# Optimization experiments

Measured on AMD Instinct MI355X. Metric: run time of the kernel, lower is better.

The kernel has to match this reference:

```python
import jax, jax.numpy as jnp
import numpy as np

N_USERS = 100_000
N_ITEMS = 50_000
N_EDGES = 2_000_000
D = 64
ALPHA = 0.5      # tanh-blend coefficient (alpha)
NORM_2 = -1.0    # exponent on back-aggregation degree norm (args.norm_2)


def setup_inputs() -> dict:
    key = jax.random.key(0)
    k1, k2, k3, k4, k5 = jax.random.split(key, 5)
    return {
        "h_user": jax.random.normal(k1, (N_USERS, D), jnp.float32) * 0.1,
        "pretrained_feature": jax.random.normal(k2, (N_ITEMS, D), jnp.float32),
        "edge_w": jax.random.normal(k3, (N_ITEMS, 1), jnp.float32),
        "src_idx": jax.random.randint(k4, (N_EDGES,), 0, N_USERS, dtype=jnp.int32),
        "dst_idx": jax.random.randint(k5, (N_EDGES,), 0, N_ITEMS, dtype=jnp.int32),
    }


def reference(h_user, pretrained_feature, edge_w, src_idx, dst_idx):
    # HGCNLayer.forward: bidirectional copy_src+sum aggregation with degree norm,
    # tanh prompt blend and node-softmax edge weighting.
    ones = jnp.ones((N_EDGES,), h_user.dtype)

    # forward pass user -> item: rst[d] = sum_{(s,d) in E} h_user[s]
    rst = jax.ops.segment_sum(h_user[src_idx], dst_idx, num_segments=N_ITEMS)  # [N_ITEMS, D]
    deg_dst = jnp.clip(jax.ops.segment_sum(ones, dst_idx, num_segments=N_ITEMS), 1.0)

    # alpha * tanh prompt blend
    rst = rst + ALPHA * jnp.tanh(pretrained_feature)
    # edge-prompt softmax scaling (softmax over nodes; see notes)
    rst = jax.nn.softmax(edge_w, axis=0) * rst
    # in-degree^-1 normalization
    rst = rst / deg_dst[:, None]

    # backward pass item -> user: bsrc[s] = sum_{(s,d) in E} rst[d]
    bsrc = jax.ops.segment_sum(rst[dst_idx], src_idx, num_segments=N_USERS)  # [N_USERS, D]
    deg_src = jnp.clip(jax.ops.segment_sum(ones, src_idx, num_segments=N_USERS), 1.0)
    bsrc = bsrc * jnp.power(deg_src, NORM_2)[:, None]
    return bsrc
```

## Files before the change

kernel.cpp:

```cpp
#include <hip/hip_runtime.h>
#include <hip/hip_bf16.h>
#include <math.h>

#define N_USERS 100000
#define N_ITEMS 50000
#define N_EDGES 2000000
#define D 64

#define SEG_SH 14
#define FSEG 8
#define BSEG 4
#define FB2 (98 * FSEG)
#define BB2 (196 * BSEG)
#define NB2 (FB2 + BB2)
#define CHUNK 16384
#define NCHUNK ((N_EDGES + CHUNK - 1) / CHUNK)
#define FWD_WGS 782
#define BWD_WGS 1563
#define CAPC 1024

__device__ __forceinline__ float blo(unsigned u) {
    union { unsigned i; float f; } c; c.i = u << 16; return c.f;
}
__device__ __forceinline__ float bhi(unsigned u) {
    union { unsigned i; float f; } c; c.i = u & 0xFFFF0000u; return c.f;
}
__device__ __forceinline__ unsigned bpack(float x, float y) {
    __hip_bfloat16 a = __float2bfloat16(x), b = __float2bfloat16(y);
    unsigned short ua = *reinterpret_cast<unsigned short*>(&a);
    unsigned short ub = *reinterpret_cast<unsigned short*>(&b);
    return (unsigned)ua | ((unsigned)ub << 16);
}

__global__ __launch_bounds__(256) void h2b_kernel(
    const float2* __restrict__ in, unsigned* __restrict__ out, int n) {
    int stride = gridDim.x * blockDim.x;
    for (int i = blockIdx.x * blockDim.x + threadIdx.x; i < n; i += stride) {
        float2 v = in[i];
        out[i] = bpack(v.x, v.y);
    }
}

__global__ __launch_bounds__(256) void hist_kernel(
    const int* __restrict__ src, const int* __restrict__ dst, int* __restrict__ gh) {
    __shared__ int h[NB2];
    for (int i = threadIdx.x; i < NB2; i += 256) h[i] = 0;
    __syncthreads();
    int stride = gridDim.x * blockDim.x;
    for (int e = blockIdx.x * blockDim.x + threadIdx.x; e < N_EDGES; e += stride) {
        int s = src[e], d = dst[e];
        atomicAdd(&h[(d >> 9) * FSEG + (s >> SEG_SH)], 1);
        atomicAdd(&h[FB2 + (s >> 9) * BSEG + (d >> SEG_SH)], 1);
    }
    __syncthreads();
    for (int i = threadIdx.x; i < NB2; i += 256) {
        int v = h[i];
        if (v) atomicAdd(&gh[i], v);
    }
}

__global__ void scan_excl(const int* __restrict__ in, int* __restrict__ out,
                          int* __restrict__ cur, int n) {
    const int T = 1024, E = 4;
    __shared__ int wsum[16];
    __shared__ int s_carry;
    if (threadIdx.x == 0) s_carry = 0;
    __syncthreads();

    int lane = threadIdx.x & 63;
    int wid  = threadIdx.x >> 6;

    for (int base = 0; base < n; base += T * E) {
        int idx0 = base + threadIdx.x * E;
        int v[E];
        int tot = 0;
#pragma unroll
        for (int e = 0; e < E; e++) {
            int i = idx0 + e;
            v[e] = (i < n) ? in[i] : 0;
            tot += v[e];
        }
        int incl = tot;
#pragma unroll
        for (int off = 1; off < 64; off <<= 1) {
            int t = __shfl_up(incl, off);
            if (lane >= off) incl += t;
        }
        if (lane == 63) wsum[wid] = incl;
        __syncthreads();
        if (wid == 0 && lane < 16) {
            int t = wsum[lane];
            int sc = t;
#pragma unroll
            for (int off = 1; off < 16; off <<= 1) {
                int u = __shfl_up(sc, off);
                if (lane >= off) sc += u;
            }
            wsum[lane] = sc - t;
        }
        __syncthreads();
        int wave_off = wsum[wid];
        int excl = s_carry + wave_off + incl - tot;
#pragma unroll
        for (int e = 0; e < E; e++) {
            int i = idx0 + e;
            if (i < n) { out[i] = excl; cur[i] = excl; }
            excl += v[e];
        }
        __syncthreads();
        if (threadIdx.x == T - 1) s_carry += wave_off + incl;
        __syncthreads();
    }
    if (threadIdx.x == 0) out[n] = s_carry;
}

__global__ __launch_bounds__(256) void binfill_kernel(
    const int* __restrict__ src, const int* __restrict__ dst,
    int* __restrict__ gcur, unsigned* __restrict__ stage) {
    __shared__ int cnt[NB2];
    __shared__ int gbase[NB2];
    __shared__ int lcur[NB2];
    int base = blockIdx.x * CHUNK;
    int nE = N_EDGES - base; if (nE > CHUNK) nE = CHUNK;

    for (int t = threadIdx.x; t < NB2; t += 256) { cnt[t] = 0; lcur[t] = 0; }
    __syncthreads();

    for (int k = threadIdx.x; k < nE; k += 256) {
        int s = src[base + k], d = dst[base + k];
        atomicAdd(&cnt[(d >> 9) * FSEG + (s >> SEG_SH)], 1);
        atomicAdd(&cnt[FB2 + (s >> 9) * BSEG + (d >> SEG_SH)], 1);
    }
    __syncthreads();
    for (int t = threadIdx.x; t < NB2; t += 256) {
        int cv = cnt[t];
        gbase[t] = cv ? atomicAdd(&gcur[t], cv) : 0;
    }
    __syncthreads();
    for (int k = threadIdx.x; k < nE; k += 256) {
        int s = src[base + k], d = dst[base + k];
        int bf = (d >> 9) * FSEG + (s >> SEG_SH);
        int p = atomicAdd(&lcur[bf], 1);
        stage[gbase[bf] + p] = (unsigned)s | ((unsigned)(d & 511) << 17);
        int bb = FB2 + (s >> 9) * BSEG + (d >> SEG_SH);
        int q2 = atomicAdd(&lcur[bb], 1);
        stage[gbase[bb] + q2] = (unsigned)d | ((unsigned)(s & 511) << 16);
    }
}

__global__ void softmax_stats_kernel(const float* __restrict__ w, float* __restrict__ stats) {
    __shared__ float red[16];
    int tid = threadIdx.x, lane = tid & 63, wid = tid >> 6;

    float m = -INFINITY;
    for (int i = tid; i < N_ITEMS; i += 1024) m = fmaxf(m, w[i]);
#pragma unroll
    for (int off = 32; off; off >>= 1) m = fmaxf(m, __shfl_xor(m, off));
    if (lane == 0) red[wid] = m;
    __syncthreads();
    if (tid == 0) {
        float t = red[0];
        for (int k = 1; k < 16; k++) t = fmaxf(t, red[k]);
        red[0] = t;
    }
    __syncthreads();
    m = red[0];
    __syncthreads();

    float s = 0.f;
    for (int i = tid; i < N_ITEMS; i += 1024) s += expf(w[i] - m);
#pragma unroll
    for (int off = 32; off; off >>= 1) s += __shfl_xor(s, off);
    if (lane == 0) red[wid] = s;
    __syncthreads();
    if (tid == 0) {
        float t = 0.f;
        for (int k = 0; k < 16; k++) t += red[k];
        stats[0] = m;
        stats[1] = t;
    }
}

__global__ __launch_bounds__(512) void pass2_fwd_kernel(
    const unsigned* __restrict__ hu16, const float* __restrict__ pf,
    const float* __restrict__ edge_w, const unsigned* __restrict__ stage,
    const int* __restrict__ binoff, const float* __restrict__ stats,
    unsigned* __restrict__ rst16) {
    __shared__ int cnt[64];
    __shared__ int loc[65];
    __shared__ int lcur[64];
    __shared__ int sorted[CAPC];
    int r = blockIdx.x;
    int B = r >> 3, sub = r & 7;
    int tid = threadIdx.x, lane = tid & 63, wv = tid >> 6;
    int q = lane & 31, half = lane >> 5;

    float ax[8], ay[8];
    int dg[8];
#pragma unroll
    for (int j = 0; j < 8; j++) { ax[j] = 0.f; ay[j] = 0.f; dg[j] = 0; }

    for (int seg = 0; seg < FSEG; seg++) {
        int cbeg = binoff[B * FSEG + seg], cend = binoff[B * FSEG + seg + 1];
        if (cbeg == cend) continue;
        if (tid < 64) { cnt[tid] = 0; lcur[tid] = 0; }
        __syncthreads();
        for (int k = cbeg + tid; k < cend; k += 512) {
            unsigned e = stage[k];
            if ((int)(e >> 23) == sub) atomicAdd(&cnt[(e >> 17) & 63], 1);
        }
        __syncthreads();
        if (tid < 64) {
            int v = cnt[tid];
            int incl = v;
#pragma unroll
            for (int off = 1; off < 64; off <<= 1) {
                int t = __shfl_up(incl, off);
                if (tid >= off) incl += t;
            }
            loc[tid] = incl - v;
            if (tid == 63) loc[64] = incl;
        }
        __syncthreads();
        int nf = loc[64];

        if (nf <= CAPC) {
            for (int k = cbeg + tid; k < cend; k += 512) {
                unsigned e = stage[k];
                if ((int)(e >> 23) == sub) {
                    int il = (e >> 17) & 63;
                    int p = atomicAdd(&lcur[il], 1);
                    sorted[loc[il] + p] = (int)(e & 0x1FFFFu);
                }
            }
            __syncthreads();
#pragma unroll
            for (int j = 0; j < 8; j++) {
                int il = wv + 8 * j;
                int a = loc[il], b = loc[il + 1];
                dg[j] += b - a;
                int k = a;
                for (; k + 4 <= b; k += 4) {
                    int s0 = sorted[k + half], s1 = sorted[k + 2 + half];
                    unsigned u0 = hu16[(s0 << 5) + q];
                    unsigned u1 = hu16[(s1 << 5) + q];
                    ax[j] += blo(u0) + blo(u1);
                    ay[j] += bhi(u0) + bhi(u1);
                }
                for (; k + 2 <= b; k += 2) {
                    unsigned u = hu16[(sorted[k + half] << 5) + q];
                    ax[j] += blo(u); ay[j] += bhi(u);
                }
                if (k < b && half == 0) {
                    unsigned u = hu16[(sorted[k] << 5) + q];
                    ax[j] += blo(u); ay[j] += bhi(u);
                }
            }
            __syncthreads();
        } else {
#pragma unroll
            for (int j = 0; j < 8; j++) {
                int il = wv + 8 * j;
                unsigned want = ((unsigned)sub << 6) | (unsigned)il;
                for (int k = cbeg; k < cend; k++) {
                    unsigned e = stage[k];
                    if ((e >> 17) == want) {
                        dg[j]++;
                        if (half == 0) {
                            unsigned u = hu16[((e & 0x1FFFFu) << 5) + q];
                            ax[j] += blo(u); ay[j] += bhi(u);
                        }
                    }
                }
            }
            __syncthreads();
        }
    }

    float m = stats[0], ssum = stats[1];
    const float2* PF2 = (const float2*)pf;
#pragma unroll
    for (int j = 0; j < 8; j++) {
        int il = wv + 8 * j;
        int i = r * 64 + il;
        if (i >= N_ITEMS) continue;
        ax[j] += __shfl_xor(ax[j], 32);
        ay[j] += __shfl_xor(ay[j], 32);
        if (half == 0) {
            float deg = (float)dg[j];
            if (deg < 1.f) deg = 1.f;
            float sc = expf(edge_w[i] - m) / (ssum * deg);
            float2 pv = PF2[(size_t)i * 32 + q];
            float vx = (ax[j] + 0.5f * tanhf(pv.x)) * sc;
            float vy = (ay[j] + 0.5f * tanhf(pv.y)) * sc;
            rst16[(size_t)i * 32 + q] = bpack(vx, vy);
        }
    }
}

__global__ __launch_bounds__(512) void pass2_bwd_kernel(
    const unsigned* __restrict__ rst16, const unsigned* __restrict__ stage,
    const int* __restrict__ binoff, float* __restrict__ out) {
    __shared__ int cnt[64];
    __shared__ int loc[65];
    __shared__ int lcur[64];
    __shared__ int sorted[CAPC];
    int r = blockIdx.x;
    int B = r >> 3, sub = r & 7;
    int tid = threadIdx.x, lane = tid & 63, wv = tid >> 6;
    int q = lane & 31, half = lane >> 5;

    float ax[8], ay[8];
    int dg[8];
#pragma unroll
    for (int j = 0; j < 8; j++) { ax[j] = 0.f; ay[j] = 0.f; dg[j] = 0; }

    for (int seg = 0; seg < BSEG; seg++) {
        int cbeg = binoff[FB2 + B * BSEG + seg], cend = binoff[FB2 + B * BSEG + seg + 1];
        if (cbeg == cend) continue;
        if (tid < 64) { cnt[tid] = 0; lcur[tid] = 0; }
        __syncthreads();
        for (int k = cbeg + tid; k < cend; k += 512) {
            unsigned e = stage[k];
            if ((int)(e >> 22) == sub) atomicAdd(&cnt[(e >> 16) & 63], 1);
        }
        __syncthreads();
        if (tid < 64) {
            int v = cnt[tid];
            int incl = v;
#pragma unroll
            for (int off = 1; off < 64; off <<= 1) {
                int t = __shfl_up(incl, off);
                if (tid >= off) incl += t;
            }
            loc[tid] = incl - v;
            if (tid == 63) loc[64] = incl;
        }
        __syncthreads();
        int nf = loc[64];

        if (nf <= CAPC) {
            for (int k = cbeg + tid; k < cend; k += 512) {
                unsigned e = stage[k];
                if ((int)(e >> 22) == sub) {
                    int il = (e >> 16) & 63;
                    int p = atomicAdd(&lcur[il], 1);
                    sorted[loc[il] + p] = (int)(e & 0xFFFFu);
                }
            }
            __syncthreads();
#pragma unroll
            for (int j = 0; j < 8; j++) {
                int il = wv + 8 * j;
                int a = loc[il], b = loc[il + 1];
                dg[j] += b - a;
                int k = a;
                for (; k + 4 <= b; k += 4) {
                    int d0 = sorted[k + half], d1 = sorted[k + 2 + half];
                    unsigned u0 = rst16[(d0 << 5) + q];
                    unsigned u1 = rst16[(d1 << 5) + q];
                    ax[j] += blo(u0) + blo(u1);
                    ay[j] += bhi(u0) + bhi(u1);
                }
                for (; k + 2 <= b; k += 2) {
                    unsigned u = rst16[(sorted[k + half] << 5) + q];
                    ax[j] += blo(u); ay[j] += bhi(u);
                }
                if (k < b && half == 0) {
                    unsigned u = rst16[(sorted[k] << 5) + q];
                    ax[j] += blo(u); ay[j] += bhi(u);
                }
            }
            __syncthreads();
        } else {
#pragma unroll
            for (int j = 0; j < 8; j++) {
                int il = wv + 8 * j;
                unsigned want = ((unsigned)sub << 6) | (unsigned)il;
                for (int k = cbeg; k < cend; k++) {
                    unsigned e = stage[k];
                    if ((e >> 16) == want) {
                        dg[j]++;
                        if (half == 0) {
                            unsigned u = rst16[((e & 0xFFFFu) << 5) + q];
                            ax[j] += blo(u); ay[j] += bhi(u);
                        }
                    }
                }
            }
            __syncthreads();
        }
    }

    float2* OUT2 = (float2*)out;
#pragma unroll
    for (int j = 0; j < 8; j++) {
        int il = wv + 8 * j;
        int u = r * 64 + il;
        if (u >= N_USERS) continue;
        ax[j] += __shfl_xor(ax[j], 32);
        ay[j] += __shfl_xor(ay[j], 32);
        if (half == 0) {
            float deg = (float)dg[j];
            if (deg < 1.f) deg = 1.f;
            OUT2[(size_t)u * 32 + q] = make_float2(ax[j] / deg, ay[j] / deg);
        }
    }
}

extern "C" void kernel_launch(void* const* d_in, const int* in_sizes, int n_in,
                              void* d_out, int out_size, void* d_ws, size_t ws_size,
                              hipStream_t stream) {
    const float* h_user = (const float*)d_in[0];
    const float* pf     = (const float*)d_in[1];
    const float* edge_w = (const float*)d_in[2];
    const int*   src    = (const int*)d_in[3];
    const int*   dst    = (const int*)d_in[4];
    float* out = (float*)d_out;

    char* p = (char*)d_ws;
    int* gh     = (int*)p;      p += sizeof(int) * NB2;
    int* binoff = (int*)p;      p += sizeof(int) * (NB2 + 1);
    int* gcur   = (int*)p;      p += sizeof(int) * NB2;
    unsigned* stage = (unsigned*)p; p += sizeof(unsigned) * (size_t)2 * N_EDGES;
    unsigned* hu16  = (unsigned*)p; p += sizeof(unsigned) * (size_t)N_USERS * 32;
    unsigned* rst16 = (unsigned*)p; p += sizeof(unsigned) * (size_t)N_ITEMS * 32;
    float* stats = (float*)p;   p += 2 * sizeof(float);

    hipMemsetAsync(gh, 0, sizeof(int) * NB2, stream);

    hist_kernel<<<256, 256, 0, stream>>>(src, dst, gh);
    scan_excl<<<1, 1024, 0, stream>>>(gh, binoff, gcur, NB2);
    binfill_kernel<<<NCHUNK, 256, 0, stream>>>(src, dst, gcur, stage);
    h2b_kernel<<<1024, 256, 0, stream>>>((const float2*)h_user, hu16, N_USERS * 32);
    softmax_stats_kernel<<<1, 1024, 0, stream>>>(edge_w, stats);
    pass2_fwd_kernel<<<FWD_WGS, 512, 0, stream>>>(hu16, pf, edge_w, stage, binoff, stats, rst16);
    pass2_bwd_kernel<<<BWD_WGS, 512, 0, stream>>>(rst16, stage, binoff, out);
}
```

Baseline: 366.7 us.

## Add refine kernel to sort bins by node once, reuse offsets in passes

Adds a refine kernel that counting-sorts each coarse bin by its 512-node local index in shared memory and writes per-node offsets. The forward and backward aggregation kernels then read contiguous per-node edge ranges instead of each of the 8 sub-blocks rescanning the whole bin, filtering and re-sorting it. This removes redundant reads of the staged edges (8x per bin) at the cost of one extra kernel launch, an extra read/write pass over the stage buffer, and a new offset array.

```diff
diff --git a/kernel.cpp b/kernel.cpp
--- a/kernel.cpp
+++ b/kernel.cpp
@@ -17,7 +17,8 @@
 #define NCHUNK ((N_EDGES + CHUNK - 1) / CHUNK)
 #define FWD_WGS 782
 #define BWD_WGS 1563
-#define CAPC 1024
+#define CAPR 4096
+#define CAPP 1024
 
 __device__ __forceinline__ float blo(unsigned u) {
     union { unsigned i; float f; } c; c.i = u << 16; return c.f;
@@ -148,6 +149,62 @@
     }
 }
 
+__global__ __launch_bounds__(512) void refine_kernel(
+    unsigned* __restrict__ stage, const int* __restrict__ binoff,
+    int* __restrict__ itemoff) {
+    __shared__ unsigned ebuf[CAPR];
+    __shared__ unsigned sbuf[CAPR];
+    __shared__ int cnt[512];
+    __shared__ int loc[512];
+    __shared__ int lcur[512];
+    __shared__ int part[8];
+    int c = blockIdx.x;
+    int beg = binoff[c], end = binoff[c + 1];
+    int n = end - beg;
+    int tid = threadIdx.x, lane = tid & 63, wv = tid >> 6;
+    int sh = (c < FB2) ? 17 : 16;
+
+    if (n > CAPR) {
+        itemoff[(size_t)c * 512 + tid] = -1;
+        return;
+    }
+
+    cnt[tid] = 0; lcur[tid] = 0;
+    for (int k = tid; k < n; k += 512) ebuf[k] = stage[beg + k];
+    __syncthreads();
+    for (int k = tid; k < n; k += 512)
+        atomicAdd(&cnt[(ebuf[k] >> sh) & 511], 1);
+    __syncthreads();
+    {
+        int v = cnt[tid];
+        int incl = v;
+#pragma unroll
+        for (int off = 1; off < 64; off <<= 1) {
+            int t = __shfl_up(incl, off);
+            if (lane >= off) incl += t;
+        }
+        if (lane == 63) part[wv] = incl;
+        __syncthreads();
+        if (tid == 0) {
+            int run = 0;
+#pragma unroll
+            for (int w = 0; w < 8; w++) { int t = part[w]; part[w] = run; run += t; }
+        }
+        __syncthreads();
+        loc[tid] = incl - v + part[wv];
+    }
+    __syncthreads();
+    for (int k = tid; k < n; k += 512) {
+        unsigned e = ebuf[k];
+        int dl = (e >> sh) & 511;
+        int p = atomicAdd(&lcur[dl], 1);
+        sbuf[loc[dl] + p] = e;
+    }
+    __syncthreads();
+    for (int k = tid; k < n; k += 512) stage[beg + k] = sbuf[k];
+    itemoff[(size_t)c * 512 + tid] = beg + loc[tid];
+}
+
 __global__ void softmax_stats_kernel(const float* __restrict__ w, float* __restrict__ stats) {
     __shared__ float red[16];
     int tid = threadIdx.x, lane = tid & 63, wid = tid >> 6;
@@ -184,14 +241,12 @@
 __global__ __launch_bounds__(512) void pass2_fwd_kernel(
     const unsigned* __restrict__ hu16, const float* __restrict__ pf,
     const float* __restrict__ edge_w, const unsigned* __restrict__ stage,
-    const int* __restrict__ binoff, const float* __restrict__ stats,
-    unsigned* __restrict__ rst16) {
-    __shared__ int cnt[64];
-    __shared__ int loc[65];
-    __shared__ int lcur[64];
-    __shared__ int sorted[CAPC];
+    const int* __restrict__ binoff, const int* __restrict__ itemoff,
+    const float* __restrict__ stats, unsigned* __restrict__ rst16) {
+    __shared__ int loc_l[65];
+    __shared__ unsigned sorted[CAPP];
     int r = blockIdx.x;
-    int B = r >> 3, sub = r & 7;
+    int B = r >> 3, g = r & 7;
     int tid = threadIdx.x, lane = tid & 63, wv = tid >> 6;
     int q = lane & 31, half = lane >> 5;
 
@@ -201,70 +256,67 @@
     for (int j = 0; j < 8; j++) { ax[j] = 0.f; ay[j] = 0.f; dg[j] = 0; }
 
     for (int seg = 0; seg < FSEG; seg++) {
-        int cbeg = binoff[B * FSEG + seg], cend = binoff[B * FSEG + seg + 1];
-        if (cbeg == cend) continue;
-        if (tid < 64) { cnt[tid] = 0; lcur[tid] = 0; }
-        __syncthreads();
-        for (int k = cbeg + tid; k < cend; k += 512) {
-            unsigned e = stage[k];
-            if ((int)(e >> 23) == sub) atomicAdd(&cnt[(e >> 17) & 63], 1);
-        }
-        __syncthreads();
-        if (tid < 64) {
-            int v = cnt[tid];
-            int incl = v;
-#pragma unroll
-            for (int off = 1; off < 64; off <<= 1) {
-                int t = __shfl_up(incl, off);
-                if (tid >= off) incl += t;
+        int c = B * FSEG + seg;
+        if (tid <= 64) {
+            int dl = g * 64 + tid;
+            loc_l[tid] = (dl == 512) ? binoff[c + 1] : itemoff[(size_t)c * 512 + dl];
+        }
+        __syncthreads();
+        if (loc_l[0] >= 0) {
+            int loc0 = loc_l[0];
+            int n = loc_l[64] - loc0;
+            if (n <= CAPP) {
+                for (int k = tid; k < n; k += 512) sorted[k] = stage[loc0 + k];
+                __syncthreads();
+#pragma unroll
+                for (int j = 0; j < 8; j++) {
+                    int il = wv + 8 * j;
+                    int a = loc_l[il] - loc0, b = loc_l[il + 1] - loc0;
+                    dg[j] += b - a;
+                    int k = a;
+                    for (; k + 4 <= b; k += 4) {
+                        int s0 = (int)(sorted[k + half] & 0x1FFFFu);
+                        int s1 = (int)(sorted[k + 2 + half] & 0x1FFFFu);
+                        unsigned u0 = hu16[(s0 << 5) + q];
+                        unsigned u1 = hu16[(s1 << 5) + q];
+                        ax[j] += blo(u0) + blo(u1);
+                        ay[j] += bhi(u0) + bhi(u1);
+                    }
+                    for (; k + 2 <= b; k += 2) {
+                        unsigned u = hu16[((sorted[k + half] & 0x1FFFFu) << 5) + q];
+                        ax[j] += blo(u); ay[j] += bhi(u);
+                    }
+                    if (k < b && half == 0) {
+                        unsigned u = hu16[((sorted[k] & 0x1FFFFu) << 5) + q];
+                        ax[j] += blo(u); ay[j] += bhi(u);
+                    }
+                }
+            } else {
+#pragma unroll
+                for (int j = 0; j < 8; j++) {
+                    int il = wv + 8 * j;
+                    int a = loc_l[il], b = loc_l[il + 1];
+                    dg[j] += b - a;
+                    int k = a;
+                    for (; k + 2 <= b; k += 2) {
+                        unsigned u = hu16[((stage[k + half] & 0x1FFFFu) << 5) + q];
+                        ax[j] += blo(u); ay[j] += bhi(u);
+                    }
+                    if (k < b && half == 0) {
+                        unsigned u = hu16[((stage[k] & 0x1FFFFu) << 5) + q];
+                        ax[j] += blo(u); ay[j] += bhi(u);
+                    }
+                }
             }
-            loc[tid] = incl - v;
-            if (tid == 63) loc[64] = incl;
-        }
-        __syncthreads();
-        int nf = loc[64];
-
-        if (nf <= CAPC) {
-            for (int k = cbeg + tid; k < cend; k += 512) {
-                unsigned e = stage[k];
-                if ((int)(e >> 23) == sub) {
-                    int il = (e >> 17) & 63;
-                    int p = atomicAdd(&lcur[il], 1);
-                    sorted[loc[il] + p] = (int)(e & 0x1FFFFu);
-                }
-            }
-            __syncthreads();
+        } else {
+            int cbeg = binoff[c], cend = binoff[c + 1];
 #pragma unroll
             for (int j = 0; j < 8; j++) {
                 int il = wv + 8 * j;
-                int a = loc[il], b = loc[il + 1];
-                dg[j] += b - a;
-                int k = a;
-                for (; k + 4 <= b; k += 4) {
-                    int s0 = sorted[k + half], s1 = sorted[k + 2 + half];
-                    unsigned u0 = hu16[(s0 << 5) + q];
-                    unsigned u1 = hu16[(s1 << 5) + q];
-                    ax[j] += blo(u0) + blo(u1);
-                    ay[j] += bhi(u0) + bhi(u1);
-                }
-                for (; k + 2 <= b; k += 2) {
-                    unsigned u = hu16[(sorted[k + half] << 5) + q];
-                    ax[j] += blo(u); ay[j] += bhi(u);
-                }
-                if (k < b && half == 0) {
-                    unsigned u = hu16[(sorted[k] << 5) + q];
-                    ax[j] += blo(u); ay[j] += bhi(u);
-                }
-            }
-            __syncthreads();
-        } else {
-#pragma unroll
-            for (int j = 0; j < 8; j++) {
-                int il = wv + 8 * j;
-                unsigned want = ((unsigned)sub << 6) | (unsigned)il;
+                unsigned want = ((unsigned)g << 6) | (unsigned)il;
                 for (int k = cbeg; k < cend; k++) {
                     unsigned e = stage[k];
-                    if ((e >> 17) == want) {
+                    if (((e >> 17) & 511u) == want) {
                         dg[j]++;
                         if (half == 0) {
                             unsigned u = hu16[((e & 0x1FFFFu) << 5) + q];
@@ -273,8 +325,8 @@
                     }
                 }
             }
-            __syncthreads();
-        }
+        }
+        __syncthreads();
     }
 
     float m = stats[0], ssum = stats[1];
@@ -300,13 +352,12 @@
 
 __global__ __launch_bounds__(512) void pass2_bwd_kernel(
     const unsigned* __restrict__ rst16, const unsigned* __restrict__ stage,
-    const int* __restrict__ binoff, float* __restrict__ out) {
-    __shared__ int cnt[64];
-    __shared__ int loc[65];
-    __shared__ int lcur[64];
-    __shared__ int sorted[CAPC];
+    const int* __restrict__ binoff, const int* __restrict__ itemoff,
+    float* __restrict__ out) {
+    __shared__ int loc_l[65];
+    __shared__ unsigned sorted[CAPP];
     int r = blockIdx.x;
-    int B = r >> 3, sub = r & 7;
+    int B = r >> 3, g = r & 7;
     int tid = threadIdx.x, lane = tid & 63, wv = tid >> 6;
     int q = lane & 31, half = lane >> 5;
 
@@ -316,70 +367,67 @@
     for (int j = 0; j < 8; j++) { ax[j] = 0.f; ay[j] = 0.f; dg[j] = 0; }
 
     for (int seg = 0; seg < BSEG; seg++) {
-        int cbeg = binoff[FB2 + B * BSEG + seg], cend = binoff[FB2 + B * BSEG + seg + 1];
-        if (cbeg == cend) continue;
-        if (tid < 64) { cnt[tid] = 0; lcur[tid] = 0; }
-        __syncthreads();
-        for (int k = cbeg + tid; k < cend; k += 512) {
-            unsigned e = stage[k];
-            if ((int)(e >> 22) == sub) atomicAdd(&cnt[(e >> 16) & 63], 1);
-        }
-        __syncthreads();
-        if (tid < 64) {
-            int v = cnt[tid];
-            int incl = v;
-#pragma unroll
-            for (int off = 1; off < 64; off <<= 1) {
-                int t = __shfl_up(incl, off);
-                if (tid >= off) incl += t;
+        int c = FB2 + B * BSEG + seg;
+        if (tid <= 64) {
+            int dl = g * 64 + tid;
+            loc_l[tid] = (dl == 512) ? binoff[c + 1] : itemoff[(size_t)c * 512 + dl];
+        }
+        __syncthreads();
+        if (loc_l[0] >= 0) {
+            int loc0 = loc_l[0];
+            int n = loc_l[64] - loc0;
+            if (n <= CAPP) {
+                for (int k = tid; k < n; k += 512) sorted[k] = stage[loc0 + k];
+                __syncthreads();
+#pragma unroll
+                for (int j = 0; j < 8; j++) {
+                    int il = wv + 8 * j;
+                    int a = loc_l[il] - loc0, b = loc_l[il + 1] - loc0;
+                    dg[j] += b - a;
+                    int k = a;
+                    for (; k + 4 <= b; k += 4) {
+                        int d0 = (int)(sorted[k + half] & 0xFFFFu);
+                        int d1 = (int)(sorted[k + 2 + half] & 0xFFFFu);
+                        unsigned u0 = rst16[(d0 << 5) + q];
+                        unsigned u1 = rst16[(d1 << 5) + q];
+                        ax[j] += blo(u0) + blo(u1);
+                        ay[j] += bhi(u0) + bhi(u1);
+                    }
+                    for (; k + 2 <= b; k += 2) {
+                        unsigned u = rst16[((sorted[k + half] & 0xFFFFu) << 5) + q];
+                        ax[j] += blo(u); ay[j] += bhi(u);
+                    }
+                    if (k < b && half == 0) {
+                        unsigned u = rst16[((sorted[k] & 0xFFFFu) << 5) + q];
+                        ax[j] += blo(u); ay[j] += bhi(u);
+                    }
+                }
+            } else {
+#pragma unroll
+                for (int j = 0; j < 8; j++) {
+                    int il = wv + 8 * j;
+                    int a = loc_l[il], b = loc_l[il + 1];
+                    dg[j] += b - a;
+                    int k = a;
+                    for (; k + 2 <= b; k += 2) {
+                        unsigned u = rst16[((stage[k + half] & 0xFFFFu) << 5) + q];
+                        ax[j] += blo(u); ay[j] += bhi(u);
+                    }
+                    if (k < b && half == 0) {
+                        unsigned u = rst16[((stage[k] & 0xFFFFu) << 5) + q];
+                        ax[j] += blo(u); ay[j] += bhi(u);
+                    }
+                }
             }
-            loc[tid] = incl - v;
-            if (tid == 63) loc[64] = incl;
-        }
-        __syncthreads();
-        int nf = loc[64];
-
-        if (nf <= CAPC) {
-            for (int k = cbeg + tid; k < cend; k += 512) {
-                unsigned e = stage[k];
-                if ((int)(e >> 22) == sub) {
-                    int il = (e >> 16) & 63;
-                    int p = atomicAdd(&lcur[il], 1);
-                    sorted[loc[il] + p] = (int)(e & 0xFFFFu);
-                }
-            }
-            __syncthreads();
+        } else {
+            int cbeg = binoff[c], cend = binoff[c + 1];
 #pragma unroll
             for (int j = 0; j < 8; j++) {
                 int il = wv + 8 * j;
-                int a = loc[il], b = loc[il + 1];
-                dg[j] += b - a;
-                int k = a;
-                for (; k + 4 <= b; k += 4) {
-                    int d0 = sorted[k + half], d1 = sorted[k + 2 + half];
-                    unsigned u0 = rst16[(d0 << 5) + q];
-                    unsigned u1 = rst16[(d1 << 5) + q];
-                    ax[j] += blo(u0) + blo(u1);
-                    ay[j] += bhi(u0) + bhi(u1);
-                }
-                for (; k + 2 <= b; k += 2) {
-                    unsigned u = rst16[(sorted[k + half] << 5) + q];
-                    ax[j] += blo(u); ay[j] += bhi(u);
-                }
-                if (k < b && half == 0) {
-                    unsigned u = rst16[(sorted[k] << 5) + q];
-                    ax[j] += blo(u); ay[j] += bhi(u);
-                }
-            }
-            __syncthreads();
-        } else {
-#pragma unroll
-            for (int j = 0; j < 8; j++) {
-                int il = wv + 8 * j;
-                unsigned want = ((unsigned)sub << 6) | (unsigned)il;
+                unsigned want = ((unsigned)g << 6) | (unsigned)il;
                 for (int k = cbeg; k < cend; k++) {
                     unsigned e = stage[k];
-                    if ((e >> 16) == want) {
+                    if (((e >> 16) & 511u) == want) {
                         dg[j]++;
                         if (half == 0) {
                             unsigned u = rst16[((e & 0xFFFFu) << 5) + q];
@@ -388,8 +436,8 @@
                     }
                 }
             }
-            __syncthreads();
-        }
+        }
+        __syncthreads();
     }
 
     float2* OUT2 = (float2*)out;
@@ -419,10 +467,11 @@
     float* out = (float*)d_out;
 
     char* p = (char*)d_ws;
-    int* gh     = (int*)p;      p += sizeof(int) * NB2;
-    int* binoff = (int*)p;      p += sizeof(int) * (NB2 + 1);
-    int* gcur   = (int*)p;      p += sizeof(int) * NB2;
+    int* gh      = (int*)p;     p += sizeof(int) * NB2;
+    int* binoff  = (int*)p;     p += sizeof(int) * (NB2 + 1);
+    int* gcur    = (int*)p;     p += sizeof(int) * NB2;
     unsigned* stage = (unsigned*)p; p += sizeof(unsigned) * (size_t)2 * N_EDGES;
+    int* itemoff = (int*)p;     p += sizeof(int) * (size_t)NB2 * 512;
     unsigned* hu16  = (unsigned*)p; p += sizeof(unsigned) * (size_t)N_USERS * 32;
     unsigned* rst16 = (unsigned*)p; p += sizeof(unsigned) * (size_t)N_ITEMS * 32;
     float* stats = (float*)p;   p += 2 * sizeof(float);
@@ -432,8 +481,9 @@
     hist_kernel<<<256, 256, 0, stream>>>(src, dst, gh);
     scan_excl<<<1, 1024, 0, stream>>>(gh, binoff, gcur, NB2);
     binfill_kernel<<<NCHUNK, 256, 0, stream>>>(src, dst, gcur, stage);
+    refine_kernel<<<NB2, 512, 0, stream>>>(stage, binoff, itemoff);
     h2b_kernel<<<1024, 256, 0, stream>>>((const float2*)h_user, hu16, N_USERS * 32);
     softmax_stats_kernel<<<1, 1024, 0, stream>>>(edge_w, stats);
-    pass2_fwd_kernel<<<FWD_WGS, 512, 0, stream>>>(hu16, pf, edge_w, stage, binoff, stats, rst16);
-    pass2_bwd_kernel<<<BWD_WGS, 512, 0, stream>>>(rst16, stage, binoff, out);
-}
+    pass2_fwd_kernel<<<FWD_WGS, 512, 0, stream>>>(hu16, pf, edge_w, stage, binoff, itemoff, stats, rst16);
+    pass2_bwd_kernel<<<BWD_WGS, 512, 0, stream>>>(rst16, stage, binoff, itemoff, out);
+}
```

After: 413.9 us. 1.13x slower.
